# Kernel tuning notes

Hardware: AMD Instinct MI355X
Metric: run time of the kernel (lower is better)

## Reference

```python
import jax, jax.numpy as jnp
import numpy as np

B, N, R, NF, NH = 2, 2048, 16384, 128, 3
PSTEP = 3


def _lin(x, w, b):
    return x @ w + b


def _mlp2(x, w0, b0, w1, b1):
    return jax.nn.relu(_lin(jax.nn.relu(_lin(x, w0, b0)), w1, b1))


def setup_inputs() -> dict:
    key = jax.random.key(0)
    ks = jax.random.split(key, 16)

    def w(k, i, o):
        return (jax.random.normal(k, (i, o), dtype=jnp.float32) / np.float32(np.sqrt(i)))

    a_cur = jax.random.uniform(ks[0], (B, N), dtype=jnp.float32)
    s_cur = jax.random.normal(ks[1], (B, N, 3), dtype=jnp.float32)
    s_delta = jax.random.normal(ks[2], (B, NH, N, 3), dtype=jnp.float32)
    # Rr/Rs: dense one-hot receiver/sender matrices (B, rel_num, N)
    Rr = jax.nn.one_hot(jax.random.randint(ks[3], (B, R), 0, N), N, dtype=jnp.float32)
    Rs = jax.nn.one_hot(jax.random.randint(ks[4], (B, R), 0, N), N, dtype=jnp.float32)
    edge_attrs = (jax.random.uniform(ks[5], (B, R, 1)) > 0.5).astype(jnp.float32)
    z = lambda n: jnp.zeros((n,), dtype=jnp.float32)
    return {
        "a_cur": a_cur, "s_cur": s_cur, "s_delta": s_delta,
        "Rr": Rr, "Rs": Rs, "edge_attrs": edge_attrs,
        "pe_w0": w(ks[6], 3 * NH + 1, NF), "pe_b0": z(NF),
        "pe_w1": w(ks[7], NF, NF), "pe_b1": z(NF),
        "re_w0": w(ks[8], 6, NF), "re_b0": z(NF),
        "re_w1": w(ks[9], NF, NF), "re_b1": z(NF),
        "re_w2": w(ks[10], NF, NF), "re_b2": z(NF),
        "rp_w": w(ks[11], 3 * NF, NF), "rp_b": z(NF),
        "pp_w": w(ks[12], 2 * NF, NF), "pp_b": z(NF),
        "pr_w0": w(ks[13], NF, NF), "pr_b0": z(NF),
        "pr_w1": w(ks[14], NF, 3), "pr_b1": z(3),
    }


def reference(a_cur, s_cur, s_delta, Rr, Rs, edge_attrs,
              pe_w0, pe_b0, pe_w1, pe_b1,
              re_w0, re_b0, re_w1, re_b1, re_w2, re_b2,
              rp_w, rp_b, pp_w, pp_b,
              pr_w0, pr_b0, pr_w1, pr_b1):
    b, nh, n, _ = s_delta.shape
    # (B, n_history, N, 3) -> (B, N, 3*n_history)
    s_delta_flat = jnp.transpose(s_delta, (0, 2, 1, 3)).reshape(b, n, -1)
    a_r = jnp.einsum('brn,bn->br', Rr, a_cur)[..., None]
    a_s = jnp.einsum('brn,bn->br', Rs, a_cur)[..., None]
    s_r = jnp.einsum('brn,bnd->brd', Rr, s_cur)
    s_s = jnp.einsum('brn,bnd->brd', Rs, s_cur)

    particle_encode = _mlp2(jnp.concatenate([s_delta_flat, a_cur[..., None]], -1),
                            pe_w0, pe_b0, pe_w1, pe_b1)
    rel_in = jnp.concatenate([a_r, a_s, s_r - s_s, edge_attrs], -1)
    relation_encode = jax.nn.relu(_lin(
        jax.nn.relu(_lin(jax.nn.relu(_lin(rel_in, re_w0, re_b0)), re_w1, re_b1)),
        re_w2, re_b2))

    effect = particle_encode
    for _ in range(PSTEP):
        e_r = jnp.einsum('brn,bnf->brf', Rr, effect)
        e_s = jnp.einsum('brn,bnf->brf', Rs, effect)
        e_rel = jax.nn.relu(_lin(jnp.concatenate([relation_encode, e_r, e_s], -1), rp_w, rp_b))
        agg = jnp.einsum('brn,brf->bnf', Rr, e_rel)  # Rr^T aggregation
        effect = jax.nn.relu(
            _lin(jnp.concatenate([particle_encode, agg], -1), pp_w, pp_b) + effect)

    pred = _lin(jax.nn.relu(_lin(effect, pr_w0, pr_b0)), pr_w1, pr_b1)
    return pred + s_cur
```

## Files before the change

kernel.cpp:

```cpp
#include <hip/hip_runtime.h>
#include <hip/hip_bf16.h>
#include <stdint.h>

#define B_ 2
#define N_ 2048
#define R_ 16384
#define NF_ 128
#define NH_ 3
#define PSTEP_ 3
#define EDGES (B_ * R_)
#define NODES (B_ * N_)
#define MAXDEG 64

typedef _Float16 f16;
typedef _Float16 f16x4 __attribute__((ext_vector_type(4)));
typedef float f32x4 __attribute__((ext_vector_type(4)));

__device__ __forceinline__ void gl16(const f16* g, f16* l, int lane) {
#if defined(__has_builtin) && __has_builtin(__builtin_amdgcn_global_load_lds)
  typedef const __attribute__((address_space(1))) uint32_t* gas_t;
  typedef __attribute__((address_space(3))) uint32_t* las_t;
  __builtin_amdgcn_global_load_lds((gas_t)(const void*)g, (las_t)(void*)l, 16, 0, 0);
#else
  *(float4*)((char*)l + lane * 16) = *(const float4*)g;
#endif
}

__global__ __launch_bounds__(256) void k_extract(const float* __restrict__ Rr,
                                                 const float* __restrict__ Rs,
                                                 int* __restrict__ recv,
                                                 int* __restrict__ send) {
  const int wid = blockIdx.x * 4 + (threadIdx.x >> 6);
  const int lane = threadIdx.x & 63;
  const bool isR = wid < EDGES;
  const int row = isR ? wid : wid - EDGES;
  const float4* p = reinterpret_cast<const float4*>((isR ? Rr : Rs) + (size_t)row * N_);
  int found = 0;
  #pragma unroll 1
  for (int it = 0; it < N_ / 256; ++it) {
    const float4 v = p[it * 64 + lane];
    const int base = (it * 64 + lane) * 4;
    bool hit = false;
    if (v.x != 0.f) { found = base;     hit = true; }
    if (v.y != 0.f) { found = base + 1; hit = true; }
    if (v.z != 0.f) { found = base + 2; hit = true; }
    if (v.w != 0.f) { found = base + 3; hit = true; }
    if (__any(hit)) break;
  }
  #pragma unroll
  for (int off = 32; off > 0; off >>= 1)
    found = max(found, __shfl_down(found, off, 64));
  if (lane == 0) (isR ? recv : send)[row] = found;
}

__global__ __launch_bounds__(256) void k_convw(
    const float* __restrict__ rp_w, const float* __restrict__ re_w1,
    const float* __restrict__ re_w2,
    f16* __restrict__ rpT_h, f16* __restrict__ rpT_l,
    f16* __restrict__ re1T_h, f16* __restrict__ re1T_l,
    f16* __restrict__ re2T_h, f16* __restrict__ re2T_l,
    int* __restrict__ counts) {
  const int i = blockIdx.x * 256 + threadIdx.x;
  const int S1 = 384 * 128, S2 = S1 + 128 * 128, S3 = S2 + 128 * 128;
  if (i < S1) {
    const int k = i >> 7, n = i & 127;
    const float v = rp_w[i];
    const f16 h = (f16)v;
    rpT_h[n * 384 + k] = h; rpT_l[n * 384 + k] = (f16)(v - (float)h);
  } else if (i < S2) {
    const int j = i - S1, k = j >> 7, n = j & 127;
    const float v = re_w1[j];
    const f16 h = (f16)v;
    re1T_h[n * 128 + k] = h; re1T_l[n * 128 + k] = (f16)(v - (float)h);
  } else if (i < S3) {
    const int j = i - S2, k = j >> 7, n = j & 127;
    const float v = re_w2[j];
    const f16 h = (f16)v;
    re2T_h[n * 128 + k] = h; re2T_l[n * 128 + k] = (f16)(v - (float)h);
  } else if (i < S3 + NODES) {
    counts[i - S3] = 0;
  }
}

__global__ __launch_bounds__(256) void k_bucket(const int* __restrict__ recv,
                                                int* __restrict__ counts,
                                                int* __restrict__ bucket) {
  const int e = blockIdx.x * 256 + threadIdx.x;
  if (e >= EDGES) return;
  const int gnode = (e >> 14) * N_ + recv[e];
  const int pos = atomicAdd(&counts[gnode], 1);
  if (pos < MAXDEG) bucket[gnode * MAXDEG + pos] = e;
}

__global__ __launch_bounds__(256) void k_particle(
    const float* __restrict__ a_cur, const float* __restrict__ s_delta,
    const float* __restrict__ w0, const float* __restrict__ b0,
    const float* __restrict__ w1, const float* __restrict__ b1,
    float* __restrict__ pe, f16* __restrict__ pe_h, f16* __restrict__ pe_l) {
  __shared__ alignas(16) float w0s[10][NF_];
  __shared__ alignas(16) float wbuf[64][NF_];
  __shared__ float b0s[NF_], b1s[NF_];
  __shared__ float xs[16][10];
  __shared__ alignas(16) float hst[NF_][20];
  const int t = threadIdx.x, f = t & 127, g = t >> 7;
  const int r0 = blockIdx.x * 16;
  for (int i = t; i < 10 * NF_; i += 256) w0s[i >> 7][i & 127] = w0[i];
  if (t < NF_) { b0s[t] = b0[t]; b1s[t] = b1[t]; }
  for (int i = t; i < 16 * 10; i += 256) {
    const int r = i / 10, k = i % 10;
    const int gr = r0 + r, b = gr >> 11, n = gr & (N_ - 1);
    xs[r][k] = (k < 9)
        ? s_delta[(((size_t)b * NH_ + (k / 3)) * N_ + n) * 3 + (k % 3)]
        : a_cur[gr];
  }
  __syncthreads();
  for (int r = g * 8; r < g * 8 + 8; ++r) {
    float a1 = b0s[f];
    #pragma unroll
    for (int k = 0; k < 10; ++k) a1 = fmaf(xs[r][k], w0s[k][f], a1);
    hst[f][r] = fmaxf(a1, 0.f);
  }
  float acc[8];
  #pragma unroll
  for (int i = 0; i < 8; ++i) acc[i] = b1s[f];
  for (int h = 0; h < 2; ++h) {
    __syncthreads();
    for (int i = t; i < 64 * NF_; i += 256) wbuf[i >> 7][i & 127] = w1[h * 64 * NF_ + i];
    __syncthreads();
    for (int k = 0; k < 64; ++k) {
      const float w = wbuf[k][f];
      #pragma unroll
      for (int i = 0; i < 2; ++i) {
        const float4 x4 = *reinterpret_cast<const float4*>(&hst[h * 64 + k][g * 8 + i * 4]);
        acc[i*4+0] = fmaf(x4.x, w, acc[i*4+0]);
        acc[i*4+1] = fmaf(x4.y, w, acc[i*4+1]);
        acc[i*4+2] = fmaf(x4.z, w, acc[i*4+2]);
        acc[i*4+3] = fmaf(x4.w, w, acc[i*4+3]);
      }
    }
  }
  #pragma unroll
  for (int i = 0; i < 8; ++i) {
    const size_t idx = (size_t)(r0 + g * 8 + i) * NF_ + f;
    const float v = fmaxf(acc[i], 0.f);
    pe[idx] = v;
    const f16 h = (f16)v;
    pe_h[idx] = h; pe_l[idx] = (f16)(v - (float)h);
  }
}

__global__ __launch_bounds__(256) void k_rel1(
    const float* __restrict__ a_cur, const float* __restrict__ s_cur,
    const float* __restrict__ ea,
    const int* __restrict__ recv, const int* __restrict__ send,
    const float* __restrict__ w0, const float* __restrict__ b0,
    f16* __restrict__ h1_h, f16* __restrict__ h1_l) {
  __shared__ alignas(16) float w0s[6][NF_];
  __shared__ float bs0[NF_];
  __shared__ alignas(16) float xt[6][36];
  const int t = threadIdx.x, f = t & 127, g = t >> 7;
  const int e0 = blockIdx.x * 32;
  for (int i = t; i < 6 * NF_; i += 256) w0s[i >> 7][i & 127] = w0[i];
  if (t < NF_) bs0[t] = b0[t];
  if (t < 32) {
    const int ge = e0 + t;
    const int b = ge >> 14;
    const int rc = recv[ge], sd = send[ge];
    xt[0][t] = a_cur[(b << 11) + rc];
    xt[1][t] = a_cur[(b << 11) + sd];
    #pragma unroll
    for (int d = 0; d < 3; ++d)
      xt[2 + d][t] = s_cur[(size_t)((b << 11) + rc) * 3 + d]
                   - s_cur[(size_t)((b << 11) + sd) * 3 + d];
    xt[5][t] = ea[ge];
  }
  __syncthreads();
  float acc[16];
  #pragma unroll
  for (int i = 0; i < 16; ++i) acc[i] = bs0[f];
  #pragma unroll
  for (int k = 0; k < 6; ++k) {
    const float w = w0s[k][f];
    #pragma unroll
    for (int i = 0; i < 4; ++i) {
      const float4 x4 = *reinterpret_cast<const float4*>(&xt[k][g * 16 + i * 4]);
      acc[i*4+0] = fmaf(x4.x, w, acc[i*4+0]);
      acc[i*4+1] = fmaf(x4.y, w, acc[i*4+1]);
      acc[i*4+2] = fmaf(x4.z, w, acc[i*4+2]);
      acc[i*4+3] = fmaf(x4.w, w, acc[i*4+3]);
    }
  }
  #pragma unroll
  for (int i = 0; i < 16; ++i) {
    const size_t idx = (size_t)(e0 + g * 16 + i) * NF_ + f;
    const float v = fmaxf(acc[i], 0.f);
    const f16 h = (f16)v;
    h1_h[idx] = h; h1_l[idx] = (f16)(v - (float)h);
  }
}

__global__ __launch_bounds__(256, 1) void k_gemm128(
    const f16* __restrict__ Ah_g, const f16* __restrict__ Al_g,
    const f16* __restrict__ Bh_g, const f16* __restrict__ Bl_g,
    const float* __restrict__ bias,
    f16* __restrict__ Ch, f16* __restrict__ Cl) {
  __shared__ f16 Ah[128 * 128], Al[128 * 128], Bh[128 * 128], Bl[128 * 128];
  const int t = threadIdx.x, lane = t & 63, w = t >> 6;
  const int l16 = lane & 15, l4 = lane >> 4;
  const size_t brow = (size_t)blockIdx.x * 128;
  #pragma unroll
  for (int rb = 0; rb < 32; rb += 4) {
    const int r0 = w * 32 + rb;
    const int row = r0 + l4;
    const int sc = (l16 ^ (row & 7)) * 8;
    gl16(Ah_g + (brow + row) * 128 + sc, &Ah[r0 * 128], lane);
    gl16(Al_g + (brow + row) * 128 + sc, &Al[r0 * 128], lane);
    gl16(Bh_g + (size_t)row * 128 + sc, &Bh[r0 * 128], lane);
    gl16(Bl_g + (size_t)row * 128 + sc, &Bl[r0 * 128], lane);
  }
  float bv[2];
  bv[0] = bias[w * 32 + l16];
  bv[1] = bias[w * 32 + 16 + l16];
  f32x4 acc[8][2];
  #pragma unroll
  for (int m = 0; m < 8; ++m)
    #pragma unroll
    for (int nf = 0; nf < 2; ++nf)
      acc[m][nf] = (f32x4){bv[nf], bv[nf], bv[nf], bv[nf]};
  __syncthreads();
  #pragma unroll 1
  for (int kk = 0; kk < 8; ++kk) {
    const int c16 = kk * 2 + (l4 >> 1);
    const int sub = (l4 & 1) * 4;
    f16x4 bh[2], bl[2];
    #pragma unroll
    for (int nf = 0; nf < 2; ++nf) {
      const int n = w * 32 + nf * 16 + l16;
      const int off = n * 128 + (c16 ^ (n & 7)) * 8 + sub;
      bh[nf] = *(const f16x4*)&Bh[off];
      bl[nf] = *(const f16x4*)&Bl[off];
    }
    #pragma unroll
    for (int m = 0; m < 8; ++m) {
      const int r = m * 16 + l16;
      const int off = r * 128 + (c16 ^ (r & 7)) * 8 + sub;
      const f16x4 ah = *(const f16x4*)&Ah[off];
      const f16x4 al = *(const f16x4*)&Al[off];
      #pragma unroll
      for (int nf = 0; nf < 2; ++nf) {
        acc[m][nf] = __builtin_amdgcn_mfma_f32_16x16x16f16(ah, bh[nf], acc[m][nf], 0, 0, 0);
        acc[m][nf] = __builtin_amdgcn_mfma_f32_16x16x16f16(ah, bl[nf], acc[m][nf], 0, 0, 0);
        acc[m][nf] = __builtin_amdgcn_mfma_f32_16x16x16f16(al, bh[nf], acc[m][nf], 0, 0, 0);
      }
    }
  }
  #pragma unroll
  for (int m = 0; m < 8; ++m)
    #pragma unroll
    for (int nf = 0; nf < 2; ++nf)
      #pragma unroll
      for (int i = 0; i < 4; ++i) {
        const float v = fmaxf(acc[m][nf][i], 0.f);
        const size_t row = brow + m * 16 + l4 * 4 + i;
        const int col = w * 32 + nf * 16 + l16;
        const f16 h = (f16)v;
        Ch[row * 128 + col] = h;
        Cl[row * 128 + col] = (f16)(v - (float)h);
      }
}

__global__ __launch_bounds__(256, 1) void k_gemm_erel(
    const f16* __restrict__ rel_h, const f16* __restrict__ rel_l,
    const f16* __restrict__ eff_h, const f16* __restrict__ eff_l,
    const int* __restrict__ recv, const int* __restrict__ send,
    const f16* __restrict__ rpT_h, const f16* __restrict__ rpT_l,
    const float* __restrict__ bias, float* __restrict__ e_rel) {
  __shared__ f16 Ah[128 * 128], Al[128 * 128], Bh[128 * 128], Bl[128 * 128];
  const int t = threadIdx.x, lane = t & 63, w = t >> 6;
  const int l16 = lane & 15, l4 = lane >> 4;
  const size_t brow = (size_t)blockIdx.x * 128;
  float bv[2];
  bv[0] = bias[w * 32 + l16];
  bv[1] = bias[w * 32 + 16 + l16];
  f32x4 acc[8][2];
  #pragma unroll
  for (int m = 0; m < 8; ++m)
    #pragma unroll
    for (int nf = 0; nf < 2; ++nf)
      acc[m][nf] = (f32x4){bv[nf], bv[nf], bv[nf], bv[nf]};
  #pragma unroll 1
  for (int ch = 0; ch < 3; ++ch) {
    if (ch) __syncthreads();
    #pragma unroll
    for (int rb = 0; rb < 32; rb += 4) {
      const int r0 = w * 32 + rb;
      const int row = r0 + l4;
      const int sc = (l16 ^ (row & 7)) * 8;
      const int ge = (int)brow + row;
      const f16 *sh, *sl; size_t aoff;
      if (ch == 0) { sh = rel_h; sl = rel_l; aoff = (size_t)ge * 128; }
      else {
        const int node = (ch == 1) ? recv[ge] : send[ge];
        sh = eff_h; sl = eff_l;
        aoff = (size_t)((ge >> 14) * N_ + node) * 128;
      }
      gl16(sh + aoff + sc, &Ah[r0 * 128], lane);
      gl16(sl + aoff + sc, &Al[r0 * 128], lane);
      gl16(rpT_h + (size_t)row * 384 + ch * 128 + sc, &Bh[r0 * 128], lane);
      gl16(rpT_l + (size_t)row * 384 + ch * 128 + sc, &Bl[r0 * 128], lane);
    }
    __syncthreads();
    #pragma unroll 1
    for (int kk = 0; kk < 8; ++kk) {
      const int c16 = kk * 2 + (l4 >> 1);
      const int sub = (l4 & 1) * 4;
      f16x4 bh[2], bl[2];
      #pragma unroll
      for (int nf = 0; nf < 2; ++nf) {
        const int n = w * 32 + nf * 16 + l16;
        const int off = n * 128 + (c16 ^ (n & 7)) * 8 + sub;
        bh[nf] = *(const f16x4*)&Bh[off];
        bl[nf] = *(const f16x4*)&Bl[off];
      }
      #pragma unroll
      for (int m = 0; m < 8; ++m) {
        const int r = m * 16 + l16;
        const int off = r * 128 + (c16 ^ (r & 7)) * 8 + sub;
        const f16x4 ah = *(const f16x4*)&Ah[off];
        const f16x4 al = *(const f16x4*)&Al[off];
        #pragma unroll
        for (int nf = 0; nf < 2; ++nf) {
          acc[m][nf] = __builtin_amdgcn_mfma_f32_16x16x16f16(ah, bh[nf], acc[m][nf], 0, 0, 0);
          acc[m][nf] = __builtin_amdgcn_mfma_f32_16x16x16f16(ah, bl[nf], acc[m][nf], 0, 0, 0);
          acc[m][nf] = __builtin_amdgcn_mfma_f32_16x16x16f16(al, bh[nf], acc[m][nf], 0, 0, 0);
        }
      }
    }
  }
  #pragma unroll
  for (int m = 0; m < 8; ++m)
    #pragma unroll
    for (int nf = 0; nf < 2; ++nf)
      #pragma unroll
      for (int i = 0; i < 4; ++i) {
        const float v = fmaxf(acc[m][nf][i], 0.f);
        const size_t row = brow + m * 16 + l4 * 4 + i;
        const int col = w * 32 + nf * 16 + l16;
        e_rel[row * 128 + col] = v;
      }
}

__global__ __launch_bounds__(256) void k_agg(
    const float* __restrict__ e_rel, const int* __restrict__ counts,
    const int* __restrict__ bucket, float* __restrict__ agg) {
  const int t = threadIdx.x, f = t & 127;
  const int gnode = blockIdx.x * 2 + (t >> 7);
  const int cnt = min(counts[gnode], MAXDEG);
  float s = 0.f;
  for (int i = 0; i < cnt; ++i) {
    const int e = bucket[gnode * MAXDEG + i];
    s += e_rel[(size_t)e * NF_ + f];
  }
  agg[(size_t)gnode * NF_ + f] = s;
}

__global__ __launch_bounds__(256) void k_update(
    const float* __restrict__ pe, const float* __restrict__ agg,
    const float* __restrict__ eff_src,
    const float* __restrict__ pp_w, const float* __restrict__ pp_b,
    float* __restrict__ eff_out, f16* __restrict__ eh, f16* __restrict__ el) {
  __shared__ alignas(16) float wbuf[64][NF_];
  __shared__ alignas(16) float xt[NF_][20];
  const int t = threadIdx.x, f = t & 127, g = t >> 7;
  const int r0 = blockIdx.x * 16;
  float acc[8];
  {
    const float bias = pp_b[f];
    #pragma unroll
    for (int i = 0; i < 8; ++i) acc[i] = bias;
  }
  for (int c = 0; c < 2; ++c) {
    __syncthreads();
    {
      const int e = t >> 4, k0 = (t & 15) * 8;
      const float* src = (c ? agg : pe) + (size_t)(r0 + e) * NF_ + k0;
      #pragma unroll
      for (int j = 0; j < 2; ++j) {
        const float4 v = *reinterpret_cast<const float4*>(src + j * 4);
        xt[k0 + j*4 + 0][e] = v.x;
        xt[k0 + j*4 + 1][e] = v.y;
        xt[k0 + j*4 + 2][e] = v.z;
        xt[k0 + j*4 + 3][e] = v.w;
      }
    }
    #pragma unroll 1
    for (int h = 0; h < 2; ++h) {
      __syncthreads();
      for (int i = t; i < 64 * NF_; i += 256)
        wbuf[i >> 7][i & 127] = pp_w[(size_t)(c * NF_ + h * 64) * NF_ + i];
      __syncthreads();
      for (int k = 0; k < 64; ++k) {
        const float w = wbuf[k][f];
        const int ka = h * 64 + k;
        #pragma unroll
        for (int i = 0; i < 2; ++i) {
          const float4 x4 = *reinterpret_cast<const float4*>(&xt[ka][g * 8 + i * 4]);
          acc[i*4+0] = fmaf(x4.x, w, acc[i*4+0]);
          acc[i*4+1] = fmaf(x4.y, w, acc[i*4+1]);
          acc[i*4+2] = fmaf(x4.z, w, acc[i*4+2]);
          acc[i*4+3] = fmaf(x4.w, w, acc[i*4+3]);
        }
      }
    }
  }
  #pragma unroll
  for (int i = 0; i < 8; ++i) {
    const size_t idx = (size_t)(r0 + g * 8 + i) * NF_ + f;
    const float v = fmaxf(acc[i] + eff_src[idx], 0.f);
    eff_out[idx] = v;
    const f16 h = (f16)v;
    eh[idx] = h; el[idx] = (f16)(v - (float)h);
  }
}

__global__ __launch_bounds__(256) void k_predict(
    const float* __restrict__ eff, const float* __restrict__ s_cur,
    const float* __restrict__ w0, const float* __restrict__ b0,
    const float* __restrict__ w1, const float* __restrict__ b1,
    float* __restrict__ out) {
  __shared__ alignas(16) float wbuf[64][NF_];
  __shared__ alignas(16) float xt[NF_][20];
  __shared__ alignas(16) float ht[NF_][20];
  __shared__ float w1s[NF_][4];
  const int t = threadIdx.x, f = t & 127, g = t >> 7;
  const int r0 = blockIdx.x * 16;
  for (int i = t; i < NF_ * 3; i += 256) w1s[i / 3][i % 3] = w1[i];
  {
    const int e = t >> 4, k0 = (t & 15) * 8;
    const float* src = eff + (size_t)(r0 + e) * NF_ + k0;
    #pragma unroll
    for (int j = 0; j < 2; ++j) {
      const float4 v = *reinterpret_cast<const float4*>(src + j * 4);
      xt[k0 + j*4 + 0][e] = v.x;
      xt[k0 + j*4 + 1][e] = v.y;
      xt[k0 + j*4 + 2][e] = v.z;
      xt[k0 + j*4 + 3][e] = v.w;
    }
  }
  float acc[8];
  {
    const float bias = b0[f];
    #pragma unroll
    for (int i = 0; i < 8; ++i) acc[i] = bias;
  }
  for (int h = 0; h < 2; ++h) {
    __syncthreads();
    for (int i = t; i < 64 * NF_; i += 256) wbuf[i >> 7][i & 127] = w0[h * 64 * NF_ + i];
    __syncthreads();
    for (int k = 0; k < 64; ++k) {
      const float w = wbuf[k][f];
      const int ka = h * 64 + k;
      #pragma unroll
      for (int i = 0; i < 2; ++i) {
        const float4 x4 = *reinterpret_cast<const float4*>(&xt[ka][g * 8 + i * 4]);
        acc[i*4+0] = fmaf(x4.x, w, acc[i*4+0]);
        acc[i*4+1] = fmaf(x4.y, w, acc[i*4+1]);
        acc[i*4+2] = fmaf(x4.z, w, acc[i*4+2]);
        acc[i*4+3] = fmaf(x4.w, w, acc[i*4+3]);
      }
    }
  }
  #pragma unroll
  for (int i = 0; i < 8; ++i) ht[f][g * 8 + i] = fmaxf(acc[i], 0.f);
  __syncthreads();
  if (t < 48) {
    const int r = t / 3, d = t % 3;
    float a2 = b1[d];
    for (int k = 0; k < NF_; ++k) a2 = fmaf(ht[k][r], w1s[k][d], a2);
    const int gr = r0 + r;
    out[(size_t)gr * 3 + d] = a2 + s_cur[(size_t)gr * 3 + d];
  }
}

extern "C" void kernel_launch(void* const* d_in, const int* in_sizes, int n_in,
                              void* d_out, int out_size, void* d_ws, size_t ws_size,
                              hipStream_t stream) {
  (void)in_sizes; (void)n_in; (void)out_size; (void)ws_size;
  const float* a_cur   = (const float*)d_in[0];
  const float* s_cur   = (const float*)d_in[1];
  const float* s_delta = (const float*)d_in[2];
  const float* Rr      = (const float*)d_in[3];
// ... 7 lines not shown
  const float* re_b0 = (const float*)d_in[11];
  const float* re_w1 = (const float*)d_in[12];
  const float* re_b1 = (const float*)d_in[13];
  const float* re_w2 = (const float*)d_in[14];
  const float* re_b2 = (const float*)d_in[15];
  const float* rp_w  = (const float*)d_in[16];
  const float* rp_b  = (const float*)d_in[17];
  const float* pp_w  = (const float*)d_in[18];
  const float* pp_b  = (const float*)d_in[19];
  const float* pr_w0 = (const float*)d_in[20];
  const float* pr_b0 = (const float*)d_in[21];
  const float* pr_w1 = (const float*)d_in[22];
  const float* pr_b1 = (const float*)d_in[23];
  float* out = (float*)d_out;

  uint8_t* wp = (uint8_t*)d_ws;
  auto alloc = [&](size_t bytes) {
    void* p = (void*)wp;
    wp += (bytes + 255) & ~(size_t)255;
    return p;
  };
  int* recv   = (int*)alloc(EDGES * 4);
  int* send   = (int*)alloc(EDGES * 4);
  int* counts = (int*)alloc(NODES * 4);
  int* bucket = (int*)alloc((size_t)NODES * MAXDEG * 4);
  float* pe   = (float*)alloc((size_t)NODES * NF_ * 4);
  f16* pe_h   = (f16*)alloc((size_t)NODES * NF_ * 2);
  f16* pe_l   = (f16*)alloc((size_t)NODES * NF_ * 2);
  float* eff  = (float*)alloc((size_t)NODES * NF_ * 4);
  f16* eff_h  = (f16*)alloc((size_t)NODES * NF_ * 2);
  f16* eff_l  = (f16*)alloc((size_t)NODES * NF_ * 2);
  float* agg  = (float*)alloc((size_t)NODES * NF_ * 4);
  f16* h1_h   = (f16*)alloc((size_t)EDGES * NF_ * 2);
  f16* h1_l   = (f16*)alloc((size_t)EDGES * NF_ * 2);
  f16* h2_h   = (f16*)alloc((size_t)EDGES * NF_ * 2);
  f16* h2_l   = (f16*)alloc((size_t)EDGES * NF_ * 2);
  f16* rel_h  = (f16*)alloc((size_t)EDGES * NF_ * 2);
  f16* rel_l  = (f16*)alloc((size_t)EDGES * NF_ * 2);
  float* e_rel = (float*)alloc((size_t)EDGES * NF_ * 4);
  f16* rpT_h  = (f16*)alloc(128 * 384 * 2);
  f16* rpT_l  = (f16*)alloc(128 * 384 * 2);
  f16* re1T_h = (f16*)alloc(128 * 128 * 2);
  f16* re1T_l = (f16*)alloc(128 * 128 * 2);
  f16* re2T_h = (f16*)alloc(128 * 128 * 2);
  f16* re2T_l = (f16*)alloc(128 * 128 * 2);

  k_extract<<<(2 * EDGES) / 4, 256, 0, stream>>>(Rr, Rs, recv, send);
  k_convw<<<(384*128 + 2*128*128 + NODES + 255) / 256, 256, 0, stream>>>(
      rp_w, re_w1, re_w2, rpT_h, rpT_l, re1T_h, re1T_l, re2T_h, re2T_l, counts);
  k_bucket<<<EDGES / 256, 256, 0, stream>>>(recv, counts, bucket);
  k_particle<<<NODES / 16, 256, 0, stream>>>(a_cur, s_delta, pe_w0, pe_b0,
                                             pe_w1, pe_b1, pe, pe_h, pe_l);
  k_rel1<<<EDGES / 32, 256, 0, stream>>>(a_cur, s_cur, ea, recv, send,
                                         re_w0, re_b0, h1_h, h1_l);
  k_gemm128<<<EDGES / 128, 256, 0, stream>>>(h1_h, h1_l, re1T_h, re1T_l,
                                             re_b1, h2_h, h2_l);
  k_gemm128<<<EDGES / 128, 256, 0, stream>>>(h2_h, h2_l, re2T_h, re2T_l,
                                             re_b2, rel_h, rel_l);

  const float* esrc = pe;
  const f16* esrc_h = pe_h;
  const f16* esrc_l = pe_l;
  for (int step = 0; step < PSTEP_; ++step) {
    k_gemm_erel<<<EDGES / 128, 256, 0, stream>>>(rel_h, rel_l, esrc_h, esrc_l,
                                                 recv, send, rpT_h, rpT_l,
                                                 rp_b, e_rel);
    k_agg<<<NODES / 2, 256, 0, stream>>>(e_rel, counts, bucket, agg);
    k_update<<<NODES / 16, 256, 0, stream>>>(pe, agg, esrc, pp_w, pp_b,
                                             eff, eff_h, eff_l);
    esrc = eff; esrc_h = eff_h; esrc_l = eff_l;
  }

  k_predict<<<NODES / 16, 256, 0, stream>>>(eff, s_cur, pr_w0, pr_b0,
                                            pr_w1, pr_b1, out);
}
```

Before: 753.8 us.

## Fuse prep kernels, chain relation-encoder MLP in LDS, scatter-add aggregation

Merges one-hot extraction, weight conversion and agg zeroing into a single prep launch. A new k_pre kernel fuses the particle encoder, the first relation layer and both relation GEMMs, so h1/h2 stay in LDS instead of going through global memory. The separate e_rel buffer, bucket sort and gather kernel are replaced by atomicAdd scatter from the edge GEMM epilogue into agg, which k_update reads and then re-zeroes. This cuts launches and global traffic at the cost of float atomics (non-deterministic summation order) and a lower-occupancy fused kernel.

```diff
diff --git a/kernel.cpp b/kernel.cpp
--- a/kernel.cpp
+++ b/kernel.cpp
@@ -10,224 +10,34 @@
 #define PSTEP_ 3
 #define EDGES (B_ * R_)
 #define NODES (B_ * N_)
-#define MAXDEG 64
+#define PREP_EXB0 1024
 
 typedef _Float16 f16;
 typedef _Float16 f16x4 __attribute__((ext_vector_type(4)));
 typedef float f32x4 __attribute__((ext_vector_type(4)));
 
-__device__ __forceinline__ void gl16(const f16* g, f16* l, int lane) {
-#if defined(__has_builtin) && __has_builtin(__builtin_amdgcn_global_load_lds)
+struct GemmLds { f16 Ah[128 * 128], Al[128 * 128], Bh[128 * 128], Bl[128 * 128]; };
+struct VecLds {
+  float wbuf[64][NF_];
+  float xt[NF_][20];
+  float ht[NF_][20];
+  float w0s[10][NF_];
+  float b0s[NF_], b1s[NF_];
+  float xs[16][10];
+  float w1s[NF_][4];
+};
+union MainLds { GemmLds g; VecLds v; };
+
+__device__ __forceinline__ void gl16(const f16* g, f16* l) {
   typedef const __attribute__((address_space(1))) uint32_t* gas_t;
   typedef __attribute__((address_space(3))) uint32_t* las_t;
   __builtin_amdgcn_global_load_lds((gas_t)(const void*)g, (las_t)(void*)l, 16, 0, 0);
-#else
-  *(float4*)((char*)l + lane * 16) = *(const float4*)g;
-#endif
-}
-
-__global__ __launch_bounds__(256) void k_extract(const float* __restrict__ Rr,
-                                                 const float* __restrict__ Rs,
-                                                 int* __restrict__ recv,
-                                                 int* __restrict__ send) {
-  const int wid = blockIdx.x * 4 + (threadIdx.x >> 6);
-  const int lane = threadIdx.x & 63;
-  const bool isR = wid < EDGES;
-  const int row = isR ? wid : wid - EDGES;
-  const float4* p = reinterpret_cast<const float4*>((isR ? Rr : Rs) + (size_t)row * N_);
-  int found = 0;
-  #pragma unroll 1
-  for (int it = 0; it < N_ / 256; ++it) {
-    const float4 v = p[it * 64 + lane];
-    const int base = (it * 64 + lane) * 4;
-    bool hit = false;
-    if (v.x != 0.f) { found = base;     hit = true; }
-    if (v.y != 0.f) { found = base + 1; hit = true; }
-    if (v.z != 0.f) { found = base + 2; hit = true; }
-    if (v.w != 0.f) { found = base + 3; hit = true; }
-    if (__any(hit)) break;
-  }
-  #pragma unroll
-  for (int off = 32; off > 0; off >>= 1)
-    found = max(found, __shfl_down(found, off, 64));
-  if (lane == 0) (isR ? recv : send)[row] = found;
-}
-
-__global__ __launch_bounds__(256) void k_convw(
-    const float* __restrict__ rp_w, const float* __restrict__ re_w1,
-    const float* __restrict__ re_w2,
-    f16* __restrict__ rpT_h, f16* __restrict__ rpT_l,
-    f16* __restrict__ re1T_h, f16* __restrict__ re1T_l,
-    f16* __restrict__ re2T_h, f16* __restrict__ re2T_l,
-    int* __restrict__ counts) {
-  const int i = blockIdx.x * 256 + threadIdx.x;
-  const int S1 = 384 * 128, S2 = S1 + 128 * 128, S3 = S2 + 128 * 128;
-  if (i < S1) {
-    const int k = i >> 7, n = i & 127;
-    const float v = rp_w[i];
-    const f16 h = (f16)v;
-    rpT_h[n * 384 + k] = h; rpT_l[n * 384 + k] = (f16)(v - (float)h);
-  } else if (i < S2) {
-    const int j = i - S1, k = j >> 7, n = j & 127;
-    const float v = re_w1[j];
-    const f16 h = (f16)v;
-    re1T_h[n * 128 + k] = h; re1T_l[n * 128 + k] = (f16)(v - (float)h);
-  } else if (i < S3) {
-    const int j = i - S2, k = j >> 7, n = j & 127;
-    const float v = re_w2[j];
-    const f16 h = (f16)v;
-    re2T_h[n * 128 + k] = h; re2T_l[n * 128 + k] = (f16)(v - (float)h);
-  } else if (i < S3 + NODES) {
-    counts[i - S3] = 0;
-  }
-}
-
-__global__ __launch_bounds__(256) void k_bucket(const int* __restrict__ recv,
-                                                int* __restrict__ counts,
-                                                int* __restrict__ bucket) {
-  const int e = blockIdx.x * 256 + threadIdx.x;
-  if (e >= EDGES) return;
-  const int gnode = (e >> 14) * N_ + recv[e];
-  const int pos = atomicAdd(&counts[gnode], 1);
-  if (pos < MAXDEG) bucket[gnode * MAXDEG + pos] = e;
-}
-
-__global__ __launch_bounds__(256) void k_particle(
-    const float* __restrict__ a_cur, const float* __restrict__ s_delta,
-    const float* __restrict__ w0, const float* __restrict__ b0,
-    const float* __restrict__ w1, const float* __restrict__ b1,
-    float* __restrict__ pe, f16* __restrict__ pe_h, f16* __restrict__ pe_l) {
-  __shared__ alignas(16) float w0s[10][NF_];
-  __shared__ alignas(16) float wbuf[64][NF_];
-  __shared__ float b0s[NF_], b1s[NF_];
-  __shared__ float xs[16][10];
-  __shared__ alignas(16) float hst[NF_][20];
-  const int t = threadIdx.x, f = t & 127, g = t >> 7;
-  const int r0 = blockIdx.x * 16;
-  for (int i = t; i < 10 * NF_; i += 256) w0s[i >> 7][i & 127] = w0[i];
-  if (t < NF_) { b0s[t] = b0[t]; b1s[t] = b1[t]; }
-  for (int i = t; i < 16 * 10; i += 256) {
-    const int r = i / 10, k = i % 10;
-    const int gr = r0 + r, b = gr >> 11, n = gr & (N_ - 1);
-    xs[r][k] = (k < 9)
-        ? s_delta[(((size_t)b * NH_ + (k / 3)) * N_ + n) * 3 + (k % 3)]
-        : a_cur[gr];
-  }
-  __syncthreads();
-  for (int r = g * 8; r < g * 8 + 8; ++r) {
-    float a1 = b0s[f];
-    #pragma unroll
-    for (int k = 0; k < 10; ++k) a1 = fmaf(xs[r][k], w0s[k][f], a1);
-    hst[f][r] = fmaxf(a1, 0.f);
-  }
-  float acc[8];
-  #pragma unroll
-  for (int i = 0; i < 8; ++i) acc[i] = b1s[f];
-  for (int h = 0; h < 2; ++h) {
-    __syncthreads();
-    for (int i = t; i < 64 * NF_; i += 256) wbuf[i >> 7][i & 127] = w1[h * 64 * NF_ + i];
-    __syncthreads();
-    for (int k = 0; k < 64; ++k) {
-      const float w = wbuf[k][f];
-      #pragma unroll
-      for (int i = 0; i < 2; ++i) {
-        const float4 x4 = *reinterpret_cast<const float4*>(&hst[h * 64 + k][g * 8 + i * 4]);
-        acc[i*4+0] = fmaf(x4.x, w, acc[i*4+0]);
-        acc[i*4+1] = fmaf(x4.y, w, acc[i*4+1]);
-        acc[i*4+2] = fmaf(x4.z, w, acc[i*4+2]);
-        acc[i*4+3] = fmaf(x4.w, w, acc[i*4+3]);
-      }
-    }
-  }
-  #pragma unroll
-  for (int i = 0; i < 8; ++i) {
-    const size_t idx = (size_t)(r0 + g * 8 + i) * NF_ + f;
-    const float v = fmaxf(acc[i], 0.f);
-    pe[idx] = v;
-    const f16 h = (f16)v;
-    pe_h[idx] = h; pe_l[idx] = (f16)(v - (float)h);
-  }
-}
-
-__global__ __launch_bounds__(256) void k_rel1(
-    const float* __restrict__ a_cur, const float* __restrict__ s_cur,
-    const float* __restrict__ ea,
-    const int* __restrict__ recv, const int* __restrict__ send,
-    const float* __restrict__ w0, const float* __restrict__ b0,
-    f16* __restrict__ h1_h, f16* __restrict__ h1_l) {
-  __shared__ alignas(16) float w0s[6][NF_];
-  __shared__ float bs0[NF_];
-  __shared__ alignas(16) float xt[6][36];
-  const int t = threadIdx.x, f = t & 127, g = t >> 7;
-  const int e0 = blockIdx.x * 32;
-  for (int i = t; i < 6 * NF_; i += 256) w0s[i >> 7][i & 127] = w0[i];
-  if (t < NF_) bs0[t] = b0[t];
-  if (t < 32) {
-    const int ge = e0 + t;
-    const int b = ge >> 14;
-    const int rc = recv[ge], sd = send[ge];
-    xt[0][t] = a_cur[(b << 11) + rc];
-    xt[1][t] = a_cur[(b << 11) + sd];
-    #pragma unroll
-    for (int d = 0; d < 3; ++d)
-      xt[2 + d][t] = s_cur[(size_t)((b << 11) + rc) * 3 + d]
-                   - s_cur[(size_t)((b << 11) + sd) * 3 + d];
-    xt[5][t] = ea[ge];
-  }
-  __syncthreads();
-  float acc[16];
-  #pragma unroll
-  for (int i = 0; i < 16; ++i) acc[i] = bs0[f];
-  #pragma unroll
-  for (int k = 0; k < 6; ++k) {
-    const float w = w0s[k][f];
-    #pragma unroll
-    for (int i = 0; i < 4; ++i) {
-      const float4 x4 = *reinterpret_cast<const float4*>(&xt[k][g * 16 + i * 4]);
-      acc[i*4+0] = fmaf(x4.x, w, acc[i*4+0]);
-      acc[i*4+1] = fmaf(x4.y, w, acc[i*4+1]);
-      acc[i*4+2] = fmaf(x4.z, w, acc[i*4+2]);
-      acc[i*4+3] = fmaf(x4.w, w, acc[i*4+3]);
-    }
-  }
-  #pragma unroll
-  for (int i = 0; i < 16; ++i) {
-    const size_t idx = (size_t)(e0 + g * 16 + i) * NF_ + f;
-    const float v = fmaxf(acc[i], 0.f);
-    const f16 h = (f16)v;
-    h1_h[idx] = h; h1_l[idx] = (f16)(v - (float)h);
-  }
-}
-
-__global__ __launch_bounds__(256, 1) void k_gemm128(
-    const f16* __restrict__ Ah_g, const f16* __restrict__ Al_g,
-    const f16* __restrict__ Bh_g, const f16* __restrict__ Bl_g,
-    const float* __restrict__ bias,
-    f16* __restrict__ Ch, f16* __restrict__ Cl) {
-  __shared__ f16 Ah[128 * 128], Al[128 * 128], Bh[128 * 128], Bl[128 * 128];
-  const int t = threadIdx.x, lane = t & 63, w = t >> 6;
+}
+
+__device__ __forceinline__ void mfma_block(const f16* Ah, const f16* Al,
+                                           const f16* Bh, const f16* Bl,
+                                           f32x4 (&acc)[8][2], int lane, int w) {
   const int l16 = lane & 15, l4 = lane >> 4;
-  const size_t brow = (size_t)blockIdx.x * 128;
-  #pragma unroll
-  for (int rb = 0; rb < 32; rb += 4) {
-    const int r0 = w * 32 + rb;
-    const int row = r0 + l4;
-    const int sc = (l16 ^ (row & 7)) * 8;
-    gl16(Ah_g + (brow + row) * 128 + sc, &Ah[r0 * 128], lane);
-    gl16(Al_g + (brow + row) * 128 + sc, &Al[r0 * 128], lane);
-    gl16(Bh_g + (size_t)row * 128 + sc, &Bh[r0 * 128], lane);
-    gl16(Bl_g + (size_t)row * 128 + sc, &Bl[r0 * 128], lane);
-  }
-  float bv[2];
-  bv[0] = bias[w * 32 + l16];
-  bv[1] = bias[w * 32 + 16 + l16];
-  f32x4 acc[8][2];
-  #pragma unroll
-  for (int m = 0; m < 8; ++m)
-    #pragma unroll
-    for (int nf = 0; nf < 2; ++nf)
-      acc[m][nf] = (f32x4){bv[nf], bv[nf], bv[nf], bv[nf]};
-  __syncthreads();
   #pragma unroll 1
   for (int kk = 0; kk < 8; ++kk) {
     const int c16 = kk * 2 + (l4 >> 1);
@@ -236,14 +46,14 @@
     #pragma unroll
     for (int nf = 0; nf < 2; ++nf) {
       const int n = w * 32 + nf * 16 + l16;
-      const int off = n * 128 + (c16 ^ (n & 7)) * 8 + sub;
+      const int off = n * 128 + ((c16 ^ (n & 7)) * 8) + sub;
       bh[nf] = *(const f16x4*)&Bh[off];
       bl[nf] = *(const f16x4*)&Bl[off];
     }
     #pragma unroll
     for (int m = 0; m < 8; ++m) {
       const int r = m * 16 + l16;
-      const int off = r * 128 + (c16 ^ (r & 7)) * 8 + sub;
+      const int off = r * 128 + ((c16 ^ (r & 7)) * 8) + sub;
       const f16x4 ah = *(const f16x4*)&Ah[off];
       const f16x4 al = *(const f16x4*)&Al[off];
       #pragma unroll
@@ -254,6 +64,11 @@
       }
     }
   }
+}
+
+__device__ __forceinline__ void frags_to_lds(f32x4 (&acc)[8][2], f16* Ah, f16* Al,
+                                             int lane, int w) {
+  const int l16 = lane & 15, l4 = lane >> 4;
   #pragma unroll
   for (int m = 0; m < 8; ++m)
     #pragma unroll
@@ -261,114 +76,289 @@
       #pragma unroll
       for (int i = 0; i < 4; ++i) {
         const float v = fmaxf(acc[m][nf][i], 0.f);
-        const size_t row = brow + m * 16 + l4 * 4 + i;
+        const int row = m * 16 + l4 * 4 + i;
         const int col = w * 32 + nf * 16 + l16;
+        const int off = row * 128 + (((col >> 3) ^ (row & 7)) * 8) + (col & 7);
         const f16 h = (f16)v;
-        Ch[row * 128 + col] = h;
-        Cl[row * 128 + col] = (f16)(v - (float)h);
-      }
-}
-
-__global__ __launch_bounds__(256, 1) void k_gemm_erel(
+        Ah[off] = h; Al[off] = (f16)(v - (float)h);
+      }
+}
+
+__global__ __launch_bounds__(256) void k_prep(
+    const float* __restrict__ Rr, const float* __restrict__ Rs,
+    const float* __restrict__ rp_w, const float* __restrict__ re_w1,
+    const float* __restrict__ re_w2,
+    int* __restrict__ recv, int* __restrict__ send,
+    f16* __restrict__ rpT_h, f16* __restrict__ rpT_l,
+    f16* __restrict__ re1T_h, f16* __restrict__ re1T_l,
+    f16* __restrict__ re2T_h, f16* __restrict__ re2T_l,
+    float4* __restrict__ agg4) {
+  const int bid = blockIdx.x, t = threadIdx.x;
+  if (bid < 512) {
+    agg4[bid * 256 + t] = make_float4(0.f, 0.f, 0.f, 0.f);
+  } else if (bid >= 513 && bid < 833) {
+    const int i = (bid - 513) * 256 + t;
+    const int S1 = 384 * 128, S2 = S1 + 128 * 128, S3 = S2 + 128 * 128;
+    if (i < S1) {
+      const int k = i >> 7, n = i & 127;
+      const float v = rp_w[i];
+      const f16 h = (f16)v;
+      rpT_h[n * 384 + k] = h; rpT_l[n * 384 + k] = (f16)(v - (float)h);
+    } else if (i < S2) {
+      const int j = i - S1, k = j >> 7, n = j & 127;
+      const float v = re_w1[j];
+      const f16 h = (f16)v;
+      re1T_h[n * 128 + k] = h; re1T_l[n * 128 + k] = (f16)(v - (float)h);
+    } else if (i < S3) {
+      const int j = i - S2, k = j >> 7, n = j & 127;
+      const float v = re_w2[j];
+      const f16 h = (f16)v;
+      re2T_h[n * 128 + k] = h; re2T_l[n * 128 + k] = (f16)(v - (float)h);
+    }
+  } else if (bid >= PREP_EXB0) {
+    const int wid = (bid - PREP_EXB0) * 4 + (t >> 6);
+    const int lane = t & 63;
+    const bool isR = wid < EDGES;
+    const int row = isR ? wid : wid - EDGES;
+    const float4* p = reinterpret_cast<const float4*>((isR ? Rr : Rs) + (size_t)row * N_);
+    int found = 0;
+    #pragma unroll 1
+    for (int it = 0; it < N_ / 256; ++it) {
+      const float4 v = p[it * 64 + lane];
+      const int base = (it * 64 + lane) * 4;
+      bool hit = false;
+      if (v.x != 0.f) { found = base;     hit = true; }
+      if (v.y != 0.f) { found = base + 1; hit = true; }
+      if (v.z != 0.f) { found = base + 2; hit = true; }
+      if (v.w != 0.f) { found = base + 3; hit = true; }
+      if (__any(hit)) break;
+    }
+    #pragma unroll
+    for (int off = 32; off > 0; off >>= 1)
+      found = max(found, __shfl_down(found, off, 64));
+    if (lane == 0) (isR ? recv : send)[row] = found;
+  }
+}
+
+__global__ __launch_bounds__(256, 1) void k_pre(
+    const float* __restrict__ a_cur, const float* __restrict__ s_cur,
+    const float* __restrict__ s_delta, const float* __restrict__ ea,
+    const int* __restrict__ recv, const int* __restrict__ send,
+    const float* __restrict__ pe_w0, const float* __restrict__ pe_b0,
+    const float* __restrict__ pe_w1, const float* __restrict__ pe_b1,
+    const float* __restrict__ re_w0, const float* __restrict__ re_b0,
+    const float* __restrict__ re_b1, const float* __restrict__ re_b2,
+    const f16* __restrict__ re1T_h, const f16* __restrict__ re1T_l,
+    const f16* __restrict__ re2T_h, const f16* __restrict__ re2T_l,
+    float* __restrict__ pe, f16* __restrict__ pe_h, f16* __restrict__ pe_l,
+    f16* __restrict__ rel_h, f16* __restrict__ rel_l) {
+  __shared__ MainLds u;
+  __shared__ float xt6[6][128];
+  __shared__ float w0s6[6][128];
+  __shared__ float sb0[128];
+
+  const int bid = blockIdx.x, t = threadIdx.x;
+  const int lane = t & 63, w = t >> 6;
+  const int l16 = lane & 15, l4 = lane >> 4;
+  const int f = t & 127, g = t >> 7;
+
+  auto stageB = [&](const f16* gh, const f16* gl) {
+    #pragma unroll
+    for (int rb = 0; rb < 32; rb += 4) {
+      const int r0w = w * 32 + rb;
+      const int row = r0w + l4;
+      const int sc = (l16 ^ (row & 7)) * 8;
+      gl16(gh + (size_t)row * 128 + sc, &u.g.Bh[r0w * 128]);
+      gl16(gl + (size_t)row * 128 + sc, &u.g.Bl[r0w * 128]);
+    }
+  };
+
+  {
+    const int r0 = bid * 16;
+    for (int i = t; i < 10 * NF_; i += 256) u.v.w0s[i >> 7][i & 127] = pe_w0[i];
+    if (t < NF_) { u.v.b0s[t] = pe_b0[t]; u.v.b1s[t] = pe_b1[t]; }
+    for (int i = t; i < 160; i += 256) {
+      const int r = i / 10, k = i % 10;
+      const int gr = r0 + r, b = gr >> 11, n = gr & (N_ - 1);
+      u.v.xs[r][k] = (k < 9)
+          ? s_delta[(((size_t)b * NH_ + (k / 3)) * N_ + n) * 3 + (k % 3)]
+          : a_cur[gr];
+    }
+    __syncthreads();
+    for (int r = g * 8; r < g * 8 + 8; ++r) {
+      float a1 = u.v.b0s[f];
+      #pragma unroll
+      for (int k = 0; k < 10; ++k) a1 = fmaf(u.v.xs[r][k], u.v.w0s[k][f], a1);
+      u.v.ht[f][r] = fmaxf(a1, 0.f);
+    }
+    float acc[8];
+    #pragma unroll
+    for (int i = 0; i < 8; ++i) acc[i] = u.v.b1s[f];
+    for (int h = 0; h < 2; ++h) {
+      __syncthreads();
+      for (int i = t; i < 64 * NF_; i += 256) u.v.wbuf[i >> 7][i & 127] = pe_w1[h * 64 * NF_ + i];
+      __syncthreads();
+      for (int k = 0; k < 64; ++k) {
+        const float wv = u.v.wbuf[k][f];
+        #pragma unroll
+        for (int i = 0; i < 2; ++i) {
+          const float4 x4 = *reinterpret_cast<const float4*>(&u.v.ht[h * 64 + k][g * 8 + i * 4]);
+          acc[i*4+0] = fmaf(x4.x, wv, acc[i*4+0]);
+          acc[i*4+1] = fmaf(x4.y, wv, acc[i*4+1]);
+          acc[i*4+2] = fmaf(x4.z, wv, acc[i*4+2]);
+          acc[i*4+3] = fmaf(x4.w, wv, acc[i*4+3]);
+        }
+      }
+    }
+    #pragma unroll
+    for (int i = 0; i < 8; ++i) {
+      const size_t idx = (size_t)(r0 + g * 8 + i) * NF_ + f;
+      const float v = fmaxf(acc[i], 0.f);
+      pe[idx] = v;
+      const f16 h = (f16)v;
+      pe_h[idx] = h; pe_l[idx] = (f16)(v - (float)h);
+    }
+  }
+  __syncthreads();
+
+  {
+    const int e0 = bid * 128;
+    if (t < 128) {
+      const int ge = e0 + t, b = ge >> 14;
+      const int rc = recv[ge], sd = send[ge];
+      xt6[0][t] = a_cur[(b << 11) + rc];
+      xt6[1][t] = a_cur[(b << 11) + sd];
+      #pragma unroll
+      for (int d = 0; d < 3; ++d)
+        xt6[2 + d][t] = s_cur[(size_t)((b << 11) + rc) * 3 + d]
+                      - s_cur[(size_t)((b << 11) + sd) * 3 + d];
+      xt6[5][t] = ea[ge];
+    }
+    stageB(re1T_h, re1T_l);
+    for (int i = t; i < 6 * 128; i += 256) w0s6[i >> 7][i & 127] = re_w0[i];
+    if (t < 128) sb0[t] = re_b0[t];
+    __syncthreads();
+    {
+      float wreg[6];
+      #pragma unroll
+      for (int k = 0; k < 6; ++k) wreg[k] = w0s6[k][f];
+      const float b0v = sb0[f];
+      for (int r = g * 64; r < g * 64 + 64; ++r) {
+        float a1 = b0v;
+        #pragma unroll
+        for (int k = 0; k < 6; ++k) a1 = fmaf(xt6[k][r], wreg[k], a1);
+        a1 = fmaxf(a1, 0.f);
+        const int off = r * 128 + ((((f >> 3)) ^ (r & 7)) * 8) + (f & 7);
+        const f16 h = (f16)a1;
+        u.g.Ah[off] = h; u.g.Al[off] = (f16)(a1 - (float)h);
+      }
+    }
+    __syncthreads();
+    f32x4 acc[8][2];
+    {
+      const float bv0 = re_b1[w * 32 + l16], bv1 = re_b1[w * 32 + 16 + l16];
+      #pragma unroll
+      for (int m = 0; m < 8; ++m) {
+        acc[m][0] = (f32x4){bv0, bv0, bv0, bv0};
+        acc[m][1] = (f32x4){bv1, bv1, bv1, bv1};
+      }
+    }
+    mfma_block(u.g.Ah, u.g.Al, u.g.Bh, u.g.Bl, acc, lane, w);
+    __syncthreads();
+    frags_to_lds(acc, u.g.Ah, u.g.Al, lane, w);
+    stageB(re2T_h, re2T_l);
+    {
+      const float bv0 = re_b2[w * 32 + l16], bv1 = re_b2[w * 32 + 16 + l16];
+      #pragma unroll
+      for (int m = 0; m < 8; ++m) {
+        acc[m][0] = (f32x4){bv0, bv0, bv0, bv0};
+        acc[m][1] = (f32x4){bv1, bv1, bv1, bv1};
+      }
+    }
+    __syncthreads();
+    mfma_block(u.g.Ah, u.g.Al, u.g.Bh, u.g.Bl, acc, lane, w);
+    __syncthreads();
+    frags_to_lds(acc, u.g.Ah, u.g.Al, lane, w);
+    __syncthreads();
+    {
+      const int row = t >> 1, hf = t & 1;
+      const float4* sA = (const float4*)&u.g.Ah[row * 128 + hf * 64];
+      const float4* sL = (const float4*)&u.g.Al[row * 128 + hf * 64];
+      float4* dA = (float4*)&rel_h[(size_t)(e0 + row) * 128 + hf * 64];
+      float4* dL = (float4*)&rel_l[(size_t)(e0 + row) * 128 + hf * 64];
+      #pragma unroll
+      for (int j = 0; j < 8; ++j) { dA[j] = sA[j]; dL[j] = sL[j]; }
+    }
+  }
+}
+
+__global__ __launch_bounds__(256, 1) void k_erel(
     const f16* __restrict__ rel_h, const f16* __restrict__ rel_l,
-    const f16* __restrict__ eff_h, const f16* __restrict__ eff_l,
+    const f16* __restrict__ src_h, const f16* __restrict__ src_l,
     const int* __restrict__ recv, const int* __restrict__ send,
     const f16* __restrict__ rpT_h, const f16* __restrict__ rpT_l,
-    const float* __restrict__ bias, float* __restrict__ e_rel) {
-  __shared__ f16 Ah[128 * 128], Al[128 * 128], Bh[128 * 128], Bl[128 * 128];
-  const int t = threadIdx.x, lane = t & 63, w = t >> 6;
+    const float* __restrict__ rp_b, float* __restrict__ agg) {
+  __shared__ GemmLds u;
+  __shared__ int eidx0[128], eidx1[128];
+  const int bid = blockIdx.x, t = threadIdx.x;
+  const int lane = t & 63, w = t >> 6;
   const int l16 = lane & 15, l4 = lane >> 4;
-  const size_t brow = (size_t)blockIdx.x * 128;
-  float bv[2];
-  bv[0] = bias[w * 32 + l16];
-  bv[1] = bias[w * 32 + 16 + l16];
+  const int e0 = bid * 128;
+  const int b = bid >> 7;
+  if (t < 128) eidx0[t] = recv[e0 + t];
+  else         eidx1[t - 128] = send[e0 + t - 128];
   f32x4 acc[8][2];
+  {
+    const float bv0 = rp_b[w * 32 + l16], bv1 = rp_b[w * 32 + 16 + l16];
+    #pragma unroll
+    for (int m = 0; m < 8; ++m) {
+      acc[m][0] = (f32x4){bv0, bv0, bv0, bv0};
+      acc[m][1] = (f32x4){bv1, bv1, bv1, bv1};
+    }
+  }
+  #pragma unroll 1
+  for (int ch = 0; ch < 3; ++ch) {
+    __syncthreads();
+    #pragma unroll
+    for (int rb = 0; rb < 32; rb += 4) {
+      const int r0w = w * 32 + rb;
+      const int row = r0w + l4;
+      const int ge = e0 + row;
+      if (ch == 0) {
+        gl16(rel_h + (size_t)ge * 128 + l16 * 8, &u.Ah[r0w * 128]);
+        gl16(rel_l + (size_t)ge * 128 + l16 * 8, &u.Al[r0w * 128]);
+      } else {
+        const int node = (ch == 1) ? eidx0[row] : eidx1[row];
+        const size_t ao = ((size_t)(b << 11) + node) * 128 + ((l16 ^ (row & 7)) * 8);
+        gl16(src_h + ao, &u.Ah[r0w * 128]);
+        gl16(src_l + ao, &u.Al[r0w * 128]);
+      }
+      const int sc = (l16 ^ (row & 7)) * 8;
+      gl16(rpT_h + (size_t)row * 384 + ch * 128 + sc, &u.Bh[r0w * 128]);
+      gl16(rpT_l + (size_t)row * 384 + ch * 128 + sc, &u.Bl[r0w * 128]);
+    }
+    __syncthreads();
+    mfma_block(u.Ah, u.Al, u.Bh, u.Bl, acc, lane, w);
+  }
   #pragma unroll
   for (int m = 0; m < 8; ++m)
     #pragma unroll
     for (int nf = 0; nf < 2; ++nf)
-      acc[m][nf] = (f32x4){bv[nf], bv[nf], bv[nf], bv[nf]};
-  #pragma unroll 1
-  for (int ch = 0; ch < 3; ++ch) {
-    if (ch) __syncthreads();
-    #pragma unroll
-    for (int rb = 0; rb < 32; rb += 4) {
-      const int r0 = w * 32 + rb;
-      const int row = r0 + l4;
-      const int sc = (l16 ^ (row & 7)) * 8;
-      const int ge = (int)brow + row;
-      const f16 *sh, *sl; size_t aoff;
-      if (ch == 0) { sh = rel_h; sl = rel_l; aoff = (size_t)ge * 128; }
-      else {
-        const int node = (ch == 1) ? recv[ge] : send[ge];
-        sh = eff_h; sl = eff_l;
-        aoff = (size_t)((ge >> 14) * N_ + node) * 128;
-      }
-      gl16(sh + aoff + sc, &Ah[r0 * 128], lane);
-      gl16(sl + aoff + sc, &Al[r0 * 128], lane);
-      gl16(rpT_h + (size_t)row * 384 + ch * 128 + sc, &Bh[r0 * 128], lane);
-      gl16(rpT_l + (size_t)row * 384 + ch * 128 + sc, &Bl[r0 * 128], lane);
-    }
-    __syncthreads();
-    #pragma unroll 1
-    for (int kk = 0; kk < 8; ++kk) {
-      const int c16 = kk * 2 + (l4 >> 1);
-      const int sub = (l4 & 1) * 4;
-      f16x4 bh[2], bl[2];
-      #pragma unroll
-      for (int nf = 0; nf < 2; ++nf) {
-        const int n = w * 32 + nf * 16 + l16;
-        const int off = n * 128 + (c16 ^ (n & 7)) * 8 + sub;
-        bh[nf] = *(const f16x4*)&Bh[off];
-        bl[nf] = *(const f16x4*)&Bl[off];
-      }
-      #pragma unroll
-      for (int m = 0; m < 8; ++m) {
-        const int r = m * 16 + l16;
-        const int off = r * 128 + (c16 ^ (r & 7)) * 8 + sub;
-        const f16x4 ah = *(const f16x4*)&Ah[off];
-        const f16x4 al = *(const f16x4*)&Al[off];
-        #pragma unroll
-        for (int nf = 0; nf < 2; ++nf) {
-          acc[m][nf] = __builtin_amdgcn_mfma_f32_16x16x16f16(ah, bh[nf], acc[m][nf], 0, 0, 0);
-          acc[m][nf] = __builtin_amdgcn_mfma_f32_16x16x16f16(ah, bl[nf], acc[m][nf], 0, 0, 0);
-          acc[m][nf] = __builtin_amdgcn_mfma_f32_16x16x16f16(al, bh[nf], acc[m][nf], 0, 0, 0);
-        }
-      }
-    }
-  }
-  #pragma unroll
-  for (int m = 0; m < 8; ++m)
-    #pragma unroll
-    for (int nf = 0; nf < 2; ++nf)
       #pragma unroll
       for (int i = 0; i < 4; ++i) {
         const float v = fmaxf(acc[m][nf][i], 0.f);
-        const size_t row = brow + m * 16 + l4 * 4 + i;
+        const int row = m * 16 + l4 * 4 + i;
         const int col = w * 32 + nf * 16 + l16;
-        e_rel[row * 128 + col] = v;
-      }
-}
-
-__global__ __launch_bounds__(256) void k_agg(
-    const float* __restrict__ e_rel, const int* __restrict__ counts,
-    const int* __restrict__ bucket, float* __restrict__ agg) {
-  const int t = threadIdx.x, f = t & 127;
-  const int gnode = blockIdx.x * 2 + (t >> 7);
-  const int cnt = min(counts[gnode], MAXDEG);
-  float s = 0.f;
-  for (int i = 0; i < cnt; ++i) {
-    const int e = bucket[gnode * MAXDEG + i];
-    s += e_rel[(size_t)e * NF_ + f];
-  }
-  agg[(size_t)gnode * NF_ + f] = s;
+        const int rc = eidx0[row];
+        atomicAdd(&agg[((size_t)(b << 11) + rc) * NF_ + col], v);
+      }
 }
 
 __global__ __launch_bounds__(256) void k_update(
-    const float* __restrict__ pe, const float* __restrict__ agg,
-    const float* __restrict__ eff_src,
+    const float* __restrict__ pe, float* __restrict__ agg,
+    const float* __restrict__ src_f,
     const float* __restrict__ pp_w, const float* __restrict__ pp_b,
-    float* __restrict__ eff_out, f16* __restrict__ eh, f16* __restrict__ el) {
+    float* __restrict__ dst_f, f16* __restrict__ dst_h, f16* __restrict__ dst_l) {
   __shared__ alignas(16) float wbuf[64][NF_];
   __shared__ alignas(16) float xt[NF_][20];
   const int t = threadIdx.x, f = t & 127, g = t >> 7;
@@ -383,14 +373,19 @@
     __syncthreads();
     {
       const int e = t >> 4, k0 = (t & 15) * 8;
-      const float* src = (c ? agg : pe) + (size_t)(r0 + e) * NF_ + k0;
+      float* srcp = (float*)((c ? agg : pe) + (size_t)(r0 + e) * NF_ + k0);
       #pragma unroll
       for (int j = 0; j < 2; ++j) {
-        const float4 v = *reinterpret_cast<const float4*>(src + j * 4);
+        const float4 v = *reinterpret_cast<const float4*>(srcp + j * 4);
         xt[k0 + j*4 + 0][e] = v.x;
         xt[k0 + j*4 + 1][e] = v.y;
         xt[k0 + j*4 + 2][e] = v.z;
         xt[k0 + j*4 + 3][e] = v.w;
+      }
+      if (c == 1) {
+        #pragma unroll
+        for (int j = 0; j < 2; ++j)
+          *reinterpret_cast<float4*>(srcp + j * 4) = make_float4(0.f, 0.f, 0.f, 0.f);
       }
     }
     #pragma unroll 1
@@ -400,15 +395,15 @@
         wbuf[i >> 7][i & 127] = pp_w[(size_t)(c * NF_ + h * 64) * NF_ + i];
       __syncthreads();
       for (int k = 0; k < 64; ++k) {
-        const float w = wbuf[k][f];
+        const float wv = wbuf[k][f];
         const int ka = h * 64 + k;
         #pragma unroll
         for (int i = 0; i < 2; ++i) {
           const float4 x4 = *reinterpret_cast<const float4*>(&xt[ka][g * 8 + i * 4]);
-          acc[i*4+0] = fmaf(x4.x, w, acc[i*4+0]);
-          acc[i*4+1] = fmaf(x4.y, w, acc[i*4+1]);
-          acc[i*4+2] = fmaf(x4.z, w, acc[i*4+2]);
-          acc[i*4+3] = fmaf(x4.w, w, acc[i*4+3]);
+          acc[i*4+0] = fmaf(x4.x, wv, acc[i*4+0]);
+          acc[i*4+1] = fmaf(x4.y, wv, acc[i*4+1]);
+          acc[i*4+2] = fmaf(x4.z, wv, acc[i*4+2]);
+          acc[i*4+3] = fmaf(x4.w, wv, acc[i*4+3]);
         }
       }
     }
@@ -416,10 +411,10 @@
   #pragma unroll
   for (int i = 0; i < 8; ++i) {
     const size_t idx = (size_t)(r0 + g * 8 + i) * NF_ + f;
-    const float v = fmaxf(acc[i] + eff_src[idx], 0.f);
-    eff_out[idx] = v;
+    const float v = fmaxf(acc[i] + src_f[idx], 0.f);
+    dst_f[idx] = v;
     const f16 h = (f16)v;
-    eh[idx] = h; el[idx] = (f16)(v - (float)h);
+    dst_h[idx] = h; dst_l[idx] = (f16)(v - (float)h);
   }
 }
 
@@ -458,15 +453,15 @@
     for (int i = t; i < 64 * NF_; i += 256) wbuf[i >> 7][i & 127] = w0[h * 64 * NF_ + i];
     __syncthreads();
     for (int k = 0; k < 64; ++k) {
-      const float w = wbuf[k][f];
+      const float wv = wbuf[k][f];
       const int ka = h * 64 + k;
       #pragma unroll
       for (int i = 0; i < 2; ++i) {
         const float4 x4 = *reinterpret_cast<const float4*>(&xt[ka][g * 8 + i * 4]);
-        acc[i*4+0] = fmaf(x4.x, w, acc[i*4+0]);
-        acc[i*4+1] = fmaf(x4.y, w, acc[i*4+1]);
-        acc[i*4+2] = fmaf(x4.z, w, acc[i*4+2]);
-        acc[i*4+3] = fmaf(x4.w, w, acc[i*4+3]);
+        acc[i*4+0] = fmaf(x4.x, wv, acc[i*4+0]);
+        acc[i*4+1] = fmaf(x4.y, wv, acc[i*4+1]);
+        acc[i*4+2] = fmaf(x4.z, wv, acc[i*4+2]);
+        acc[i*4+3] = fmaf(x4.w, wv, acc[i*4+3]);
       }
     }
   }
@@ -520,8 +515,6 @@
   };
   int* recv   = (int*)alloc(EDGES * 4);
   int* send   = (int*)alloc(EDGES * 4);
-  int* counts = (int*)alloc(NODES * 4);
-  int* bucket = (int*)alloc((size_t)NODES * MAXDEG * 4);
   float* pe   = (float*)alloc((size_t)NODES * NF_ * 4);
   f16* pe_h   = (f16*)alloc((size_t)NODES * NF_ * 2);
   f16* pe_l   = (f16*)alloc((size_t)NODES * NF_ * 2);
@@ -529,13 +522,8 @@
   f16* eff_h  = (f16*)alloc((size_t)NODES * NF_ * 2);
   f16* eff_l  = (f16*)alloc((size_t)NODES * NF_ * 2);
   float* agg  = (float*)alloc((size_t)NODES * NF_ * 4);
-  f16* h1_h   = (f16*)alloc((size_t)EDGES * NF_ * 2);
-  f16* h1_l   = (f16*)alloc((size_t)EDGES * NF_ * 2);
-  f16* h2_h   = (f16*)alloc((size_t)EDGES * NF_ * 2);
-  f16* h2_l   = (f16*)alloc((size_t)EDGES * NF_ * 2);
   f16* rel_h  = (f16*)alloc((size_t)EDGES * NF_ * 2);
   f16* rel_l  = (f16*)alloc((size_t)EDGES * NF_ * 2);
-  float* e_rel = (float*)alloc((size_t)EDGES * NF_ * 4);
   f16* rpT_h  = (f16*)alloc(128 * 384 * 2);
   f16* rpT_l  = (f16*)alloc(128 * 384 * 2);
   f16* re1T_h = (f16*)alloc(128 * 128 * 2);
@@ -543,27 +531,22 @@
   f16* re2T_h = (f16*)alloc(128 * 128 * 2);
   f16* re2T_l = (f16*)alloc(128 * 128 * 2);
 
-  k_extract<<<(2 * EDGES) / 4, 256, 0, stream>>>(Rr, Rs, recv, send);
-  k_convw<<<(384*128 + 2*128*128 + NODES + 255) / 256, 256, 0, stream>>>(
-      rp_w, re_w1, re_w2, rpT_h, rpT_l, re1T_h, re1T_l, re2T_h, re2T_l, counts);
-  k_bucket<<<EDGES / 256, 256, 0, stream>>>(recv, counts, bucket);
-  k_particle<<<NODES / 16, 256, 0, stream>>>(a_cur, s_delta, pe_w0, pe_b0,
-                                             pe_w1, pe_b1, pe, pe_h, pe_l);
-  k_rel1<<<EDGES / 32, 256, 0, stream>>>(a_cur, s_cur, ea, recv, send,
-                                         re_w0, re_b0, h1_h, h1_l);
-  k_gemm128<<<EDGES / 128, 256, 0, stream>>>(h1_h, h1_l, re1T_h, re1T_l,
-                                             re_b1, h2_h, h2_l);
-  k_gemm128<<<EDGES / 128, 256, 0, stream>>>(h2_h, h2_l, re2T_h, re2T_l,
-                                             re_b2, rel_h, rel_l);
+  k_prep<<<PREP_EXB0 + (2 * EDGES) / 4, 256, 0, stream>>>(
+      Rr, Rs, rp_w, re_w1, re_w2, recv, send,
+      rpT_h, rpT_l, re1T_h, re1T_l, re2T_h, re2T_l, (float4*)agg);
+
+  k_pre<<<256, 256, 0, stream>>>(
+      a_cur, s_cur, s_delta, ea, recv, send,
+      pe_w0, pe_b0, pe_w1, pe_b1, re_w0, re_b0, re_b1, re_b2,
+      re1T_h, re1T_l, re2T_h, re2T_l,
+      pe, pe_h, pe_l, rel_h, rel_l);
 
   const float* esrc = pe;
   const f16* esrc_h = pe_h;
   const f16* esrc_l = pe_l;
-  for (int step = 0; step < PSTEP_; ++step) {
-    k_gemm_erel<<<EDGES / 128, 256, 0, stream>>>(rel_h, rel_l, esrc_h, esrc_l,
-                                                 recv, send, rpT_h, rpT_l,
-                                                 rp_b, e_rel);
-    k_agg<<<NODES / 2, 256, 0, stream>>>(e_rel, counts, bucket, agg);
+  for (int s = 0; s < PSTEP_; ++s) {
+    k_erel<<<EDGES / 128, 256, 0, stream>>>(rel_h, rel_l, esrc_h, esrc_l,
+                                            recv, send, rpT_h, rpT_l, rp_b, agg);
     k_update<<<NODES / 16, 256, 0, stream>>>(pe, agg, esrc, pp_w, pp_b,
                                              eff, eff_h, eff_l);
     esrc = eff; esrc_h = eff_h; esrc_l = eff_l;
```

New measurement: 702.1 us. -6.9%, faster.
